# Kernel tuning notes

Hardware: AMD Instinct MI355X
Metric: run time of the kernel (lower is better)

## Reference

```python
import jax, jax.numpy as jnp
import numpy as np

N, C_IN, H, W = 8, 512, 56, 56
CH = 128  # make_divisible(512*0.25, 8)
SCALE = CH ** (-0.5)
BN_EPS = 1e-5


def setup_inputs() -> dict:
    key = jax.random.key(0)
    ks = jax.random.split(key, 6)
    x = jax.random.normal(ks[0], (N, C_IN, H, W), dtype=jnp.float32)
    # 1x1 conv W: in_channels -> 3*channels (with bias)
    W_w = jax.random.normal(ks[1], (3 * CH, C_IN), dtype=jnp.float32) * (2.0 / C_IN) ** 0.5
    W_b = jnp.zeros((3 * CH,), dtype=jnp.float32)
    # 1x1 conv Z: channels -> in_channels (no bias, followed by BN)
    Z_w = jax.random.normal(ks[2], (C_IN, CH), dtype=jnp.float32) * (2.0 / CH) ** 0.5
    bn_gamma = jax.random.normal(ks[3], (C_IN,), dtype=jnp.float32) * 0.1
    bn_beta = jnp.zeros((C_IN,), dtype=jnp.float32)
    bn_mean = jnp.zeros((C_IN,), dtype=jnp.float32)
    bn_var = jnp.ones((C_IN,), dtype=jnp.float32)
    return {"x": x, "W_w": W_w, "W_b": W_b, "Z_w": Z_w,
            "bn_gamma": bn_gamma, "bn_beta": bn_beta,
            "bn_mean": bn_mean, "bn_var": bn_var}


def reference(x, W_w, W_b, Z_w, bn_gamma, bn_beta, bn_mean, bn_var):
    n, c, h, w = x.shape
    xf = x.reshape(n, c, h * w)                               # [N, C, HW]
    proj = jnp.einsum('oc,ncq->noq', W_w, xf) + W_b[None, :, None]  # [N, 3*CH, HW]
    t, p, g = jnp.split(proj, 3, axis=1)                      # each [N, CH, HW]
    s = jnp.einsum('ncq,nck->nqk', t, p)                      # [N, HW, HW]
    s = jax.nn.softmax(s * SCALE, axis=2)
    att = jnp.einsum('nqv,ncv->ncq', s, g)                    # [N, CH, HW]
    z = jnp.einsum('oc,ncq->noq', Z_w, att)                   # [N, C, HW]
    # BatchNorm2d, inference form with running stats
    inv = bn_gamma / jnp.sqrt(bn_var + BN_EPS)
    z = z * inv[None, :, None] + (bn_beta - bn_mean * inv)[None, :, None]
    return z.reshape(n, c, h, w) + x
```

## Files before the change

kernel.cpp:

```cpp
#include <hip/hip_runtime.h>
#include <hip/hip_bf16.h>
#include <math.h>

#define NB    8
#define CIN   512
#define HW    3136
#define CH    128
#define TCH   384
#define SCALE 0.08838834764831845f
#define QKSCALE 0.12751744f
#define BNEPS 1e-5f
#define NSPLIT 4
#define QB    128

typedef __attribute__((ext_vector_type(8)))  short bf16x8;
typedef __attribute__((ext_vector_type(4)))  short bf16x4;
typedef __attribute__((ext_vector_type(4)))  float f32x4;
typedef __attribute__((ext_vector_type(16))) float f32x16;

#define MFMA16(a, b, c) __builtin_amdgcn_mfma_f32_16x16x32_bf16((a), (b), (c), 0, 0, 0)
#define MFMA32(a, b, c) __builtin_amdgcn_mfma_f32_32x32x16_bf16((a), (b), (c), 0, 0, 0)

__device__ inline short f2bf(float f) {
    __hip_bfloat16 h = __float2bfloat16(f);
    return *reinterpret_cast<short*>(&h);
}
__device__ inline unsigned pack2bf(float a, float b) {
    return (unsigned)(unsigned short)f2bf(a) | ((unsigned)(unsigned short)f2bf(b) << 16);
}
__device__ inline float bfraw2f(unsigned short u) {
    return __uint_as_float(((unsigned)u) << 16);
}
__device__ inline float exp2a(float x) {
    float r; asm("v_exp_f32 %0, %1" : "=v"(r) : "v"(x)); return r;
}

__global__ __launch_bounds__(256) void cvt_wts(const float* __restrict__ Ww,
                                               const float* __restrict__ Zw,
                                               __hip_bfloat16* __restrict__ WwB,
                                               __hip_bfloat16* __restrict__ ZwB) {
    const int nW = TCH * CIN / 4;
    const int nZ = CIN * CH / 4;
    int i = blockIdx.x * 256 + threadIdx.x;
    if (i < nW) {
        float4 v = ((const float4*)Ww)[i];
        bf16x4 o; o[0] = f2bf(v.x); o[1] = f2bf(v.y); o[2] = f2bf(v.z); o[3] = f2bf(v.w);
        ((bf16x4*)WwB)[i] = o;
    } else if (i < nW + nZ) {
        int j = i - nW;
        float4 v = ((const float4*)Zw)[j];
        bf16x4 o; o[0] = f2bf(v.x); o[1] = f2bf(v.y); o[2] = f2bf(v.z); o[3] = f2bf(v.w);
        ((bf16x4*)ZwB)[j] = o;
    }
}

__global__ __launch_bounds__(256) void xpose_kernel(const float* __restrict__ x,
                                                    __hip_bfloat16* __restrict__ xT) {
    const int n = blockIdx.z, c0 = blockIdx.y * 64, q0 = blockIdx.x * 64;
    const int tid = threadIdx.x;
    const int mr = tid >> 4, mq = tid & 15;

    __shared__ char T[64 * 128];

    const float* xp = x + ((size_t)(n * CIN + c0 + mr * 4)) * HW + q0 + mq * 4;
    float4 r0 = *(const float4*)(xp);
    float4 r1 = *(const float4*)(xp + HW);
    float4 r2 = *(const float4*)(xp + 2 * HW);
    float4 r3 = *(const float4*)(xp + 3 * HW);
    const float* f0 = (const float*)&r0; const float* f1 = (const float*)&r1;
    const float* f2 = (const float*)&r2; const float* f3 = (const float*)&r3;
#pragma unroll
    for (int j = 0; j < 4; ++j) {
        int q = mq * 4 + j;
        bf16x4 v; v[0] = f2bf(f0[j]); v[1] = f2bf(f1[j]);
                  v[2] = f2bf(f2[j]); v[3] = f2bf(f3[j]);
        *(bf16x4*)(T + q * 128 + ((mr * 8) ^ ((q & 15) << 3))) = v;
    }
    __syncthreads();

    __hip_bfloat16* og = xT + ((size_t)n * HW + q0) * CIN + c0;
#pragma unroll
    for (int it = 0; it < 2; ++it) {
        int ch = it * 256 + tid, rr = ch >> 3, o8 = ch & 7;
        int sw = (rr & 15) << 3;
        bf16x4 lo = *(const bf16x4*)(T + rr * 128 + ((o8 * 16) ^ sw));
        bf16x4 hi = *(const bf16x4*)(T + rr * 128 + ((o8 * 16 + 8) ^ sw));
        bf16x8 v; v[0] = lo[0]; v[1] = lo[1]; v[2] = lo[2]; v[3] = lo[3];
                  v[4] = hi[0]; v[5] = hi[1]; v[6] = hi[2]; v[7] = hi[3];
        *(bf16x8*)(og + (size_t)rr * CIN + o8 * 8) = v;
    }
}

__global__ __launch_bounds__(256) void proj_kernel(const __hip_bfloat16* __restrict__ xT,
                                                   const __hip_bfloat16* __restrict__ WwB,
                                                   const float* __restrict__ Wb,
                                                   __hip_bfloat16* __restrict__ Qt,
                                                   __hip_bfloat16* __restrict__ Kt,
                                                   __hip_bfloat16* __restrict__ Vg) {
    const int n  = blockIdx.z;
    const int m0 = blockIdx.y * 64;
    const int q0 = blockIdx.x * 64;
    const int tid = threadIdx.x;
    const int lane = tid & 63, wv = tid >> 6;
    const int lr = lane & 15, hi = lane >> 4;

    __shared__ char Aw[64 * 128];
    __shared__ char Bx[64 * 128];
    __shared__ char Ts[64 * 128];

    f32x4 acc[4] = {};
    const __hip_bfloat16* xn = xT + ((size_t)n * HW + q0) * CIN;

    for (int k0 = 0; k0 < CIN; k0 += 64) {
#pragma unroll
        for (int it = 0; it < 2; ++it) {
            int ch = it * 256 + tid, r = ch >> 3, o = ch & 7;
            int sw = (o * 16) ^ ((r & 7) << 4);
            bf16x8 a = *(const bf16x8*)(WwB + (size_t)(m0 + r) * CIN + k0 + o * 8);
            *(bf16x8*)(Aw + r * 128 + sw) = a;
            bf16x8 b = *(const bf16x8*)(xn + (size_t)r * CIN + k0 + o * 8);
            *(bf16x8*)(Bx + r * 128 + sw) = b;
        }
        __syncthreads();

        const int mrow = wv * 16 + lr;
#pragma unroll
        for (int ks = 0; ks < 2; ++ks) {
            bf16x8 af = *(const bf16x8*)(Aw + mrow * 128 +
                                         ((ks * 64 + hi * 16) ^ ((mrow & 7) << 4)));
#pragma unroll
            for (int kn = 0; kn < 4; ++kn) {
                int qrow = kn * 16 + lr;
                bf16x8 bfr = *(const bf16x8*)(Bx + qrow * 128 +
                                              ((ks * 64 + hi * 16) ^ ((qrow & 7) << 4)));
                acc[kn] = MFMA16(af, bfr, acc[kn]);
            }
        }
        __syncthreads();
    }

    const int region = m0 >> 7;
    const int c0     = m0 & 127;
    const float oscale = (region == 0) ? QKSCALE : 1.0f;

    float bias[4];
#pragma unroll
    for (int reg = 0; reg < 4; ++reg) bias[reg] = Wb[m0 + wv * 16 + hi * 4 + reg];

#pragma unroll
    for (int kn = 0; kn < 4; ++kn)
#pragma unroll
        for (int reg = 0; reg < 4; ++reg) {
            __hip_bfloat16 v = __float2bfloat16((acc[kn][reg] + bias[reg]) * oscale);
            int row, colb;
            if (region < 2) { row = kn * 16 + lr; colb = (wv * 16 + hi * 4 + reg) * 2; }
            else            { row = wv * 16 + hi * 4 + reg; colb = (kn * 16 + lr) * 2; }
            *(__hip_bfloat16*)(Ts + row * 128 + (colb ^ ((row & 7) << 4))) = v;
        }
    __syncthreads();

    __hip_bfloat16* base;
    size_t rstride;
    if (region == 0)      { base = Qt + (size_t)n * HW * CH + (size_t)q0 * CH + c0; rstride = CH; }
    else if (region == 1) { base = Kt + (size_t)n * HW * CH + (size_t)q0 * CH + c0; rstride = CH; }
    else                  { base = Vg + (size_t)n * CH * HW + (size_t)c0 * HW + q0; rstride = HW; }

#pragma unroll
    for (int it = 0; it < 2; ++it) {
        int ch = it * 256 + tid, rr = ch >> 3, o = ch & 7;
        bf16x8 v = *(const bf16x8*)(Ts + rr * 128 + ((o * 16) ^ ((rr & 7) << 4)));
        *(bf16x8*)(base + (size_t)rr * rstride + o * 8) = v;
    }
}

__global__ __launch_bounds__(256, 2) void attn_kernel(
        const __hip_bfloat16* __restrict__ Qt,
        const __hip_bfloat16* __restrict__ Kt,
        const __hip_bfloat16* __restrict__ Vg,
        __hip_bfloat16* __restrict__ PO,
        float* __restrict__ Mbuf,
        float* __restrict__ Lbuf) {
    const int n = blockIdx.y, s = blockIdx.z;
    const int q0 = blockIdx.x * QB;
    const int tid = threadIdx.x;
    const int lane = tid & 63, wv = tid >> 6;
    const int l31 = lane & 31, h = lane >> 5;

    __shared__ char smem[32768];
    char* Ks = smem;
    char* Vt = smem + 16384;

    const int t0 = (s == 0) ? 0 : (13 + 12 * (s - 1));
    const int t1 = t0 + ((s == 0) ? 13 : 12);

    const __hip_bfloat16* Kg = Kt + (size_t)n * HW * CH;
    const __hip_bfloat16* Vp = Vg + (size_t)n * CH * HW;

    const int qg = q0 + wv * 32 + l31;
    const int qc = (qg < HW) ? qg : (HW - 1);
    const __hip_bfloat16* Qg = Qt + ((size_t)n * HW + qc) * CH + h * 8;
    bf16x8 qf[8];
#pragma unroll
    for (int cs = 0; cs < 8; ++cs) qf[cs] = *(const bf16x8*)(Qg + cs * 16);

    const int kr = tid >> 2, kgb = (tid & 3) * 4;
    const int ksz = (kr & 7) ^ (((kr >> 3) & 1) << 3);
    const int vr = tid >> 1, vgb = (tid & 1) * 4;
    const int vsz = vr & 7;
    const __hip_bfloat16* Ksrc = Kg + (size_t)kr * CH;
    const __hip_bfloat16* Vsrc = Vp + (size_t)vr * HW;
    char* Kd = Ks + kr * 256;
    char* Vd = Vt + vr * 128;

    bf16x8 kreg[4], vreg[4];
    {
        const int kk = t0 * 64;
#pragma unroll
        for (int i = 0; i < 4; ++i)
            kreg[i] = *(const bf16x8*)(Ksrc + (size_t)kk * CH + (kgb + i) * 8);
#pragma unroll
        for (int i = 0; i < 4; ++i)
            vreg[i] = *(const bf16x8*)(Vsrc + kk + (vgb + i) * 8);
    }
#pragma unroll
    for (int i = 0; i < 4; ++i) *(bf16x8*)(Kd + ((kgb + i) ^ ksz) * 16) = kreg[i];
#pragma unroll
    for (int i = 0; i < 4; ++i) *(bf16x8*)(Vd + ((vgb + i) ^ vsz) * 16) = vreg[i];
    __syncthreads();

    const int rsw = (l31 & 7) ^ (((l31 >> 3) & 1) << 3);
    const int vrsw = l31 & 7;

    f32x16 O[4] = {};
    float m_i = -1e30f, l_i = 0.f;

    for (int t = t0; t < t1; ++t) {
        if (t + 1 < t1) {
            const int kk = (t + 1) * 64;
#pragma unroll
            for (int i = 0; i < 4; ++i)
                kreg[i] = *(const bf16x8*)(Ksrc + (size_t)kk * CH + (kgb + i) * 8);
#pragma unroll
            for (int i = 0; i < 4; ++i)
                vreg[i] = *(const bf16x8*)(Vsrc + kk + (vgb + i) * 8);
        }

        f32x16 sa0 = {}, sa1 = {};
#pragma unroll
        for (int cs = 0; cs < 8; ++cs) {
            int goff = ((cs * 2 + h) ^ rsw) * 16;
            bf16x8 k0f = *(const bf16x8*)(Ks + l31 * 256 + goff);
            bf16x8 k1f = *(const bf16x8*)(Ks + (32 + l31) * 256 + goff);
            sa0 = MFMA32(k0f, qf[cs], sa0);
            sa1 = MFMA32(k1f, qf[cs], sa1);
        }

        float pmax = sa0[0];
#pragma unroll
        for (int r = 0; r < 16; ++r) {
            pmax = fmaxf(pmax, sa0[r]);
            pmax = fmaxf(pmax, sa1[r]);
        }
        pmax = fmaxf(pmax, __shfl_xor(pmax, 32));

        if (__any(pmax > m_i)) {
            float nm = fmaxf(m_i, pmax);
            float f  = exp2a(m_i - nm);
            l_i *= f; m_i = nm;
#pragma unroll
            for (int ct = 0; ct < 4; ++ct)
#pragma unroll
                for (int r = 0; r < 16; ++r) O[ct][r] *= f;
        }

        float rs = 0.f;
#pragma unroll
        for (int r = 0; r < 16; ++r) {
            sa0[r] = exp2a(sa0[r] - m_i); rs += sa0[r];
            sa1[r] = exp2a(sa1[r] - m_i); rs += sa1[r];
        }
        rs += __shfl_xor(rs, 32);
        l_i += rs;

        union { unsigned u[4]; bf16x8 v; } pf0, pf1, pf2, pf3;
        {
            unsigned w0 = pack2bf(sa0[0],  sa0[1]),  w1 = pack2bf(sa0[2],  sa0[3]);
            unsigned w2 = pack2bf(sa0[4],  sa0[5]),  w3 = pack2bf(sa0[6],  sa0[7]);
            unsigned w4 = pack2bf(sa0[8],  sa0[9]),  w5 = pack2bf(sa0[10], sa0[11]);
            unsigned w6 = pack2bf(sa0[12], sa0[13]), w7 = pack2bf(sa0[14], sa0[15]);
            unsigned x0 = __shfl_xor((int)w0, 32), x1 = __shfl_xor((int)w1, 32);
            unsigned x2 = __shfl_xor((int)w2, 32), x3 = __shfl_xor((int)w3, 32);
            unsigned x4 = __shfl_xor((int)w4, 32), x5 = __shfl_xor((int)w5, 32);
            unsigned x6 = __shfl_xor((int)w6, 32), x7 = __shfl_xor((int)w7, 32);
            pf0.u[0] = h ? x2 : w0; pf0.u[1] = h ? x3 : w1;
            pf0.u[2] = h ? w2 : x0; pf0.u[3] = h ? w3 : x1;
            pf1.u[0] = h ? x6 : w4; pf1.u[1] = h ? x7 : w5;
            pf1.u[2] = h ? w6 : x4; pf1.u[3] = h ? w7 : x5;
        }
        {
            unsigned w0 = pack2bf(sa1[0],  sa1[1]),  w1 = pack2bf(sa1[2],  sa1[3]);
            unsigned w2 = pack2bf(sa1[4],  sa1[5]),  w3 = pack2bf(sa1[6],  sa1[7]);
            unsigned w4 = pack2bf(sa1[8],  sa1[9]),  w5 = pack2bf(sa1[10], sa1[11]);
            unsigned w6 = pack2bf(sa1[12], sa1[13]), w7 = pack2bf(sa1[14], sa1[15]);
            unsigned x0 = __shfl_xor((int)w0, 32), x1 = __shfl_xor((int)w1, 32);
            unsigned x2 = __shfl_xor((int)w2, 32), x3 = __shfl_xor((int)w3, 32);
            unsigned x4 = __shfl_xor((int)w4, 32), x5 = __shfl_xor((int)w5, 32);
            unsigned x6 = __shfl_xor((int)w6, 32), x7 = __shfl_xor((int)w7, 32);
            pf2.u[0] = h ? x2 : w0; pf2.u[1] = h ? x3 : w1;
            pf2.u[2] = h ? w2 : x0; pf2.u[3] = h ? w3 : x1;
            pf3.u[0] = h ? x6 : w4; pf3.u[1] = h ? x7 : w5;
            pf3.u[2] = h ? w6 : x4; pf3.u[3] = h ? w7 : x5;
        }

#pragma unroll
        for (int ct = 0; ct < 4; ++ct) {
            const char* vrow = Vt + (ct * 32 + l31) * 128;
            bf16x8 v0 = *(const bf16x8*)(vrow + ((0 + h) ^ vrsw) * 16);
            bf16x8 v1 = *(const bf16x8*)(vrow + ((2 + h) ^ vrsw) * 16);
            bf16x8 v2 = *(const bf16x8*)(vrow + ((4 + h) ^ vrsw) * 16);
            bf16x8 v3 = *(const bf16x8*)(vrow + ((6 + h) ^ vrsw) * 16);
            O[ct] = MFMA32(v0, pf0.v, O[ct]);
            O[ct] = MFMA32(v1, pf1.v, O[ct]);
            O[ct] = MFMA32(v2, pf2.v, O[ct]);
            O[ct] = MFMA32(v3, pf3.v, O[ct]);
        }

        __syncthreads();
        if (t + 1 < t1) {
#pragma unroll
            for (int i = 0; i < 4; ++i) *(bf16x8*)(Kd + ((kgb + i) ^ ksz) * 16) = kreg[i];
#pragma unroll
            for (int i = 0; i < 4; ++i) *(bf16x8*)(Vd + ((vgb + i) ^ vsz) * 16) = vreg[i];
        }
        __syncthreads();
    }

    const int qrow = wv * 32 + l31;
    const int esw  = (qrow & 7) << 4;
#pragma unroll
    for (int ct = 0; ct < 4; ++ct)
#pragma unroll
        for (int i = 0; i < 8; ++i) {
            int c = ct * 32 + 2 * (i & 1) + 8 * (i >> 1) + 4 * h;
            unsigned u = pack2bf(O[ct][2 * i], O[ct][2 * i + 1]);
            *(unsigned*)(smem + qrow * 256 + ((c * 2) ^ esw)) = u;
        }
    __syncthreads();
    __hip_bfloat16* pg = PO + ((size_t)(s * NB + n) * HW + q0) * CH;
#pragma unroll
    for (int it = 0; it < 8; ++it) {
        int ch = it * 256 + tid, r = ch >> 4, g = ch & 15;
        if (q0 + r < HW) {
            bf16x8 v = *(const bf16x8*)(smem + r * 256 + ((g * 16) ^ ((r & 7) << 4)));
            *(bf16x8*)(pg + (size_t)r * CH + g * 8) = v;
        }
    }
    if (h == 0 && qg < HW) {
        size_t base = (size_t)(s * NB + n) * HW + qg;
        Mbuf[base] = m_i; Lbuf[base] = l_i;
    }
}

__global__ __launch_bounds__(256) void merge_kernel(
        const __hip_bfloat16* __restrict__ PO,
        const float* __restrict__ Mbuf,
        const float* __restrict__ Lbuf,
        __hip_bfloat16* __restrict__ att) {
    const int idx = blockIdx.x * 256 + threadIdx.x;
    const int nq = idx >> 4;
    const int c0 = (idx & 15) * 8;
    const size_t NHW = (size_t)NB * HW;

    float m[NSPLIT], l[NSPLIT];
#pragma unroll
    for (int s = 0; s < NSPLIT; ++s) { m[s] = Mbuf[s * NHW + nq]; l[s] = Lbuf[s * NHW + nq]; }
    float M = m[0];
#pragma unroll
    for (int s = 1; s < NSPLIT; ++s) M = fmaxf(M, m[s]);
    float w[NSPLIT], denom = 0.f;
#pragma unroll
    for (int s = 0; s < NSPLIT; ++s) { w[s] = exp2f(m[s] - M); denom += w[s] * l[s]; }
    float rinv = 1.f / denom;

    float acc[8] = {};
#pragma unroll
    for (int s = 0; s < NSPLIT; ++s) {
        union { bf16x8 v; unsigned short u[8]; } p;
        p.v = *(const bf16x8*)(PO + (size_t)s * NHW * CH + (size_t)nq * CH + c0);
#pragma unroll
        for (int j = 0; j < 8; ++j) acc[j] += w[s] * bfraw2f(p.u[j]);
    }
    union { bf16x8 v; unsigned short u[8]; } ov;
#pragma unroll
    for (int j = 0; j < 8; ++j) ov.u[j] = (unsigned short)f2bf(acc[j] * rinv);
    *(bf16x8*)(att + (size_t)nq * CH + c0) = ov.v;
}

__global__ __launch_bounds__(256) void zbn_kernel(const __hip_bfloat16* __restrict__ att,
                                                  const __hip_bfloat16* __restrict__ ZwB,
                                                  const float* __restrict__ gamma,
                                                  const float* __restrict__ beta,
                                                  const float* __restrict__ mean,
                                                  const float* __restrict__ var,
                                                  const float* __restrict__ x,
                                                  float* __restrict__ out) {
    const int n  = blockIdx.z;
    const int m0 = blockIdx.y * 64;
    const int q0 = blockIdx.x * 64;
    const int tid = threadIdx.x;
    const int lane = tid & 63, wv = tid >> 6;
    const int lr = lane & 15, hi = lane >> 4;

    __shared__ char smem[32768];
    char* Az = smem;
    char* Ba = smem + 16384;

#pragma unroll
    for (int it = 0; it < 4; ++it) {
        int ch = it * 256 + tid, r = ch >> 4, o = ch & 15;
        int sw = (o * 16) ^ ((r & 7) << 4);
        bf16x8 a = *(const bf16x8*)(ZwB + (size_t)(m0 + r) * CH + o * 8);
        *(bf16x8*)(Az + r * 256 + sw) = a;
        bf16x8 b = *(const bf16x8*)(att + ((size_t)n * HW + q0 + r) * CH + o * 8);
        *(bf16x8*)(Ba + r * 256 + sw) = b;
    }
    __syncthreads();

    f32x4 acc[4] = {};
    const int mrow = wv * 16 + lr;
#pragma unroll
    for (int ks = 0; ks < 4; ++ks) {
        bf16x8 af = *(const bf16x8*)(Az + mrow * 256 +
                                     ((ks * 64 + hi * 16) ^ ((mrow & 7) << 4)));
#pragma unroll
        for (int kn = 0; kn < 4; ++kn) {
            int qrow = kn * 16 + lr;
            bf16x8 bfr = *(const bf16x8*)(Ba + qrow * 256 +
                                          ((ks * 64 + hi * 16) ^ ((qrow & 7) << 4)));
            acc[kn] = MFMA16(af, bfr, acc[kn]);
        }
    }
    __syncthreads();

    float inv[4], add[4];
#pragma unroll
    for (int reg = 0; reg < 4; ++reg) {
        int m = m0 + wv * 16 + hi * 4 + reg;
        inv[reg] = gamma[m] * rsqrtf(var[m] + BNEPS);
        add[reg] = beta[m] - mean[m] * inv[reg];
    }

#pragma unroll
    for (int kn = 0; kn < 4; ++kn)
#pragma unroll
        for (int reg = 0; reg < 4; ++reg) {
            int row = wv * 16 + hi * 4 + reg;
            int colb = (kn * 16 + lr) * 4;
            *(float*)(smem + row * 256 + (colb ^ ((row & 7) << 4))) =
                acc[kn][reg] * inv[reg] + add[reg];
        }
    __syncthreads();

#pragma unroll
    for (int it = 0; it < 4; ++it) {
        int ch = it * 256 + tid, rr = ch >> 4, o = ch & 15;
        f32x4 v = *(const f32x4*)(smem + rr * 256 + ((o * 16) ^ ((rr & 7) << 4)));
        size_t idx = (size_t)n * CIN * HW + (size_t)(m0 + rr) * HW + q0 + o * 4;
        float4 xv = *(const float4*)(x + idx);
        float4 ov; ov.x = v[0] + xv.x; ov.y = v[1] + xv.y;
                   ov.z = v[2] + xv.z; ov.w = v[3] + xv.w;
        *(float4*)(out + idx) = ov;
    }
}

extern "C" void kernel_launch(void* const* d_in, const int* in_sizes, int n_in,
                              void* d_out, int out_size, void* d_ws, size_t ws_size,
                              hipStream_t stream) {
    const float* x     = (const float*)d_in[0];
    const float* Ww    = (const float*)d_in[1];
    const float* Wb    = (const float*)d_in[2];
    const float* Zw    = (const float*)d_in[3];
    const float* gamma = (const float*)d_in[4];
    const float* beta  = (const float*)d_in[5];
    const float* mean  = (const float*)d_in[6];
    const float* var   = (const float*)d_in[7];
    float* out = (float*)d_out;

    const size_t xT_bytes  = (size_t)NB * HW * CIN * 2;
    const size_t qkv_bytes = (size_t)NB * HW * CH * 2;
    char* ob = (char*)d_out;
    __hip_bfloat16* xT  = (__hip_bfloat16*)ob;
    __hip_bfloat16* Qt  = (__hip_bfloat16*)(ob + xT_bytes);
    __hip_bfloat16* Kt  = (__hip_bfloat16*)(ob + xT_bytes + qkv_bytes);
    __hip_bfloat16* Vgb = (__hip_bfloat16*)(ob + xT_bytes + 2 * qkv_bytes);
    __hip_bfloat16* PO  = (__hip_bfloat16*)ob;

    char* w = (char*)d_ws;
    __hip_bfloat16* attb = (__hip_bfloat16*)w;                       w += qkv_bytes;
    __hip_bfloat16* WwB  = (__hip_bfloat16*)w;                       w += (size_t)TCH * CIN * 2;
    __hip_bfloat16* ZwB  = (__hip_bfloat16*)w;                       w += (size_t)CIN * CH * 2;
    float* Mbuf = (float*)w;                                         w += (size_t)NSPLIT * NB * HW * 4;
    float* Lbuf = (float*)w;

    cvt_wts<<<dim3(256), 256, 0, stream>>>(Ww, Zw, WwB, ZwB);
    xpose_kernel<<<dim3(HW / 64, CIN / 64, NB), 256, 0, stream>>>(x, xT);
    proj_kernel<<<dim3(HW / 64, TCH / 64, NB), 256, 0, stream>>>(xT, WwB, Wb, Qt, Kt, Vgb);
    attn_kernel<<<dim3((HW + QB - 1) / QB, NB, NSPLIT), 256, 0, stream>>>(Qt, Kt, Vgb,
                                                                          PO, Mbuf, Lbuf);
    merge_kernel<<<dim3(NB * HW * 16 / 256), 256, 0, stream>>>(PO, Mbuf, Lbuf, attb);
    zbn_kernel<<<dim3(HW / 64, CIN / 64, NB), 256, 0, stream>>>(attb, ZwB, gamma, beta,
                                                                mean, var, x, out);
}
```

Before: 150.8 us.

## Widen projection tile to 128 rows, use permlane32 swap and MFMA priority in attention

The projection kernel now computes 128 output channels per block instead of 64, so each x tile loaded into shared memory is reused across twice as many MFMAs and half as many blocks are launched. In the attention loop, the cross-half shuffles used to build the P operand are replaced by v_permlane32_swap_b32, which avoids the LDS-backed shuffles and the select instructions. The MFMA sections are also wrapped in s_setprio raises so waves issuing matrix ops get scheduling priority. In exchange, the projection kernel uses more registers and LDS per block, and the epilogue is serialized over two halves with extra barriers.

```diff
diff --git a/kernel.cpp b/kernel.cpp
--- a/kernel.cpp
+++ b/kernel.cpp
@@ -98,78 +98,87 @@
                                                    __hip_bfloat16* __restrict__ Kt,
                                                    __hip_bfloat16* __restrict__ Vg) {
     const int n  = blockIdx.z;
-    const int m0 = blockIdx.y * 64;
+    const int m0 = blockIdx.y * 128;
     const int q0 = blockIdx.x * 64;
     const int tid = threadIdx.x;
     const int lane = tid & 63, wv = tid >> 6;
     const int lr = lane & 15, hi = lane >> 4;
 
-    __shared__ char Aw[64 * 128];
+    __shared__ char Aw[128 * 128];
     __shared__ char Bx[64 * 128];
     __shared__ char Ts[64 * 128];
 
-    f32x4 acc[4] = {};
+    f32x4 acc[2][4] = {};
     const __hip_bfloat16* xn = xT + ((size_t)n * HW + q0) * CIN;
 
     for (int k0 = 0; k0 < CIN; k0 += 64) {
+#pragma unroll
+        for (int it = 0; it < 4; ++it) {
+            int ch = it * 256 + tid, r = ch >> 3, o = ch & 7;
+            bf16x8 a = *(const bf16x8*)(WwB + (size_t)(m0 + r) * CIN + k0 + o * 8);
+            *(bf16x8*)(Aw + r * 128 + ((o * 16) ^ ((r & 7) << 4))) = a;
+        }
 #pragma unroll
         for (int it = 0; it < 2; ++it) {
             int ch = it * 256 + tid, r = ch >> 3, o = ch & 7;
-            int sw = (o * 16) ^ ((r & 7) << 4);
-            bf16x8 a = *(const bf16x8*)(WwB + (size_t)(m0 + r) * CIN + k0 + o * 8);
-            *(bf16x8*)(Aw + r * 128 + sw) = a;
             bf16x8 b = *(const bf16x8*)(xn + (size_t)r * CIN + k0 + o * 8);
-            *(bf16x8*)(Bx + r * 128 + sw) = b;
+            *(bf16x8*)(Bx + r * 128 + ((o * 16) ^ ((r & 7) << 4))) = b;
         }
         __syncthreads();
 
-        const int mrow = wv * 16 + lr;
 #pragma unroll
         for (int ks = 0; ks < 2; ++ks) {
-            bf16x8 af = *(const bf16x8*)(Aw + mrow * 128 +
-                                         ((ks * 64 + hi * 16) ^ ((mrow & 7) << 4)));
-#pragma unroll
-            for (int kn = 0; kn < 4; ++kn) {
-                int qrow = kn * 16 + lr;
-                bf16x8 bfr = *(const bf16x8*)(Bx + qrow * 128 +
-                                              ((ks * 64 + hi * 16) ^ ((qrow & 7) << 4)));
-                acc[kn] = MFMA16(af, bfr, acc[kn]);
+#pragma unroll
+            for (int half = 0; half < 2; ++half) {
+                const int mrow = half * 64 + wv * 16 + lr;
+                bf16x8 af = *(const bf16x8*)(Aw + mrow * 128 +
+                                             ((ks * 64 + hi * 16) ^ ((mrow & 7) << 4)));
+#pragma unroll
+                for (int kn = 0; kn < 4; ++kn) {
+                    int qrow = kn * 16 + lr;
+                    bf16x8 bfr = *(const bf16x8*)(Bx + qrow * 128 +
+                                                  ((ks * 64 + hi * 16) ^ ((qrow & 7) << 4)));
+                    acc[half][kn] = MFMA16(af, bfr, acc[half][kn]);
+                }
             }
         }
         __syncthreads();
     }
 
-    const int region = m0 >> 7;
-    const int c0     = m0 & 127;
-    const float oscale = (region == 0) ? QKSCALE : 1.0f;
-
-    float bias[4];
-#pragma unroll
-    for (int reg = 0; reg < 4; ++reg) bias[reg] = Wb[m0 + wv * 16 + hi * 4 + reg];
-
-#pragma unroll
-    for (int kn = 0; kn < 4; ++kn)
-#pragma unroll
-        for (int reg = 0; reg < 4; ++reg) {
-            __hip_bfloat16 v = __float2bfloat16((acc[kn][reg] + bias[reg]) * oscale);
-            int row, colb;
-            if (region < 2) { row = kn * 16 + lr; colb = (wv * 16 + hi * 4 + reg) * 2; }
-            else            { row = wv * 16 + hi * 4 + reg; colb = (kn * 16 + lr) * 2; }
-            *(__hip_bfloat16*)(Ts + row * 128 + (colb ^ ((row & 7) << 4))) = v;
-        }
-    __syncthreads();
-
-    __hip_bfloat16* base;
-    size_t rstride;
-    if (region == 0)      { base = Qt + (size_t)n * HW * CH + (size_t)q0 * CH + c0; rstride = CH; }
-    else if (region == 1) { base = Kt + (size_t)n * HW * CH + (size_t)q0 * CH + c0; rstride = CH; }
-    else                  { base = Vg + (size_t)n * CH * HW + (size_t)c0 * HW + q0; rstride = HW; }
-
-#pragma unroll
-    for (int it = 0; it < 2; ++it) {
-        int ch = it * 256 + tid, rr = ch >> 3, o = ch & 7;
-        bf16x8 v = *(const bf16x8*)(Ts + rr * 128 + ((o * 16) ^ ((rr & 7) << 4)));
-        *(bf16x8*)(base + (size_t)rr * rstride + o * 8) = v;
+#pragma unroll
+    for (int half = 0; half < 2; ++half) {
+        const int mbase  = m0 + half * 64;
+        const int region = mbase >> 7;
+        const int c0     = mbase & 127;
+        const float oscale = (region == 0) ? QKSCALE : 1.0f;
+
+#pragma unroll
+        for (int kn = 0; kn < 4; ++kn)
+#pragma unroll
+            for (int reg = 0; reg < 4; ++reg) {
+                float bias = Wb[mbase + wv * 16 + hi * 4 + reg];
+                __hip_bfloat16 v =
+                    __float2bfloat16((acc[half][kn][reg] + bias) * oscale);
+                int row, colb;
+                if (region < 2) { row = kn * 16 + lr; colb = (wv * 16 + hi * 4 + reg) * 2; }
+                else            { row = wv * 16 + hi * 4 + reg; colb = (kn * 16 + lr) * 2; }
+                *(__hip_bfloat16*)(Ts + row * 128 + (colb ^ ((row & 7) << 4))) = v;
+            }
+        __syncthreads();
+
+        __hip_bfloat16* base;
+        size_t rstride;
+        if (region == 0)      { base = Qt + (size_t)n * HW * CH + (size_t)q0 * CH + c0; rstride = CH; }
+        else if (region == 1) { base = Kt + (size_t)n * HW * CH + (size_t)q0 * CH + c0; rstride = CH; }
+        else                  { base = Vg + (size_t)n * CH * HW + (size_t)c0 * HW + q0; rstride = HW; }
+
+#pragma unroll
+        for (int it = 0; it < 2; ++it) {
+            int ch = it * 256 + tid, rr = ch >> 3, o = ch & 7;
+            bf16x8 v = *(const bf16x8*)(Ts + rr * 128 + ((o * 16) ^ ((rr & 7) << 4)));
+            *(bf16x8*)(base + (size_t)rr * rstride + o * 8) = v;
+        }
+        __syncthreads();
     }
 }
 
@@ -246,6 +255,7 @@
         }
 
         f32x16 sa0 = {}, sa1 = {};
+        __builtin_amdgcn_s_setprio(1);
 #pragma unroll
         for (int cs = 0; cs < 8; ++cs) {
             int goff = ((cs * 2 + h) ^ rsw) * 16;
@@ -254,6 +264,7 @@
             sa0 = MFMA32(k0f, qf[cs], sa0);
             sa1 = MFMA32(k1f, qf[cs], sa1);
         }
+        __builtin_amdgcn_s_setprio(0);
 
         float pmax = sa0[0];
 #pragma unroll
@@ -288,30 +299,27 @@
             unsigned w2 = pack2bf(sa0[4],  sa0[5]),  w3 = pack2bf(sa0[6],  sa0[7]);
             unsigned w4 = pack2bf(sa0[8],  sa0[9]),  w5 = pack2bf(sa0[10], sa0[11]);
             unsigned w6 = pack2bf(sa0[12], sa0[13]), w7 = pack2bf(sa0[14], sa0[15]);
-            unsigned x0 = __shfl_xor((int)w0, 32), x1 = __shfl_xor((int)w1, 32);
-            unsigned x2 = __shfl_xor((int)w2, 32), x3 = __shfl_xor((int)w3, 32);
-            unsigned x4 = __shfl_xor((int)w4, 32), x5 = __shfl_xor((int)w5, 32);
-            unsigned x6 = __shfl_xor((int)w6, 32), x7 = __shfl_xor((int)w7, 32);
-            pf0.u[0] = h ? x2 : w0; pf0.u[1] = h ? x3 : w1;
-            pf0.u[2] = h ? w2 : x0; pf0.u[3] = h ? w3 : x1;
-            pf1.u[0] = h ? x6 : w4; pf1.u[1] = h ? x7 : w5;
-            pf1.u[2] = h ? w6 : x4; pf1.u[3] = h ? w7 : x5;
+            asm("v_permlane32_swap_b32 %0, %1" : "+v"(w0), "+v"(w2));
+            asm("v_permlane32_swap_b32 %0, %1" : "+v"(w1), "+v"(w3));
+            asm("v_permlane32_swap_b32 %0, %1" : "+v"(w4), "+v"(w6));
+            asm("v_permlane32_swap_b32 %0, %1" : "+v"(w5), "+v"(w7));
+            pf0.u[0] = w0; pf0.u[1] = w1; pf0.u[2] = w2; pf0.u[3] = w3;
+            pf1.u[0] = w4; pf1.u[1] = w5; pf1.u[2] = w6; pf1.u[3] = w7;
         }
         {
             unsigned w0 = pack2bf(sa1[0],  sa1[1]),  w1 = pack2bf(sa1[2],  sa1[3]);
             unsigned w2 = pack2bf(sa1[4],  sa1[5]),  w3 = pack2bf(sa1[6],  sa1[7]);
             unsigned w4 = pack2bf(sa1[8],  sa1[9]),  w5 = pack2bf(sa1[10], sa1[11]);
             unsigned w6 = pack2bf(sa1[12], sa1[13]), w7 = pack2bf(sa1[14], sa1[15]);
-            unsigned x0 = __shfl_xor((int)w0, 32), x1 = __shfl_xor((int)w1, 32);
-            unsigned x2 = __shfl_xor((int)w2, 32), x3 = __shfl_xor((int)w3, 32);
-            unsigned x4 = __shfl_xor((int)w4, 32), x5 = __shfl_xor((int)w5, 32);
-            unsigned x6 = __shfl_xor((int)w6, 32), x7 = __shfl_xor((int)w7, 32);
-            pf2.u[0] = h ? x2 : w0; pf2.u[1] = h ? x3 : w1;
-            pf2.u[2] = h ? w2 : x0; pf2.u[3] = h ? w3 : x1;
-            pf3.u[0] = h ? x6 : w4; pf3.u[1] = h ? x7 : w5;
-            pf3.u[2] = h ? w6 : x4; pf3.u[3] = h ? w7 : x5;
-        }
-
+            asm("v_permlane32_swap_b32 %0, %1" : "+v"(w0), "+v"(w2));
+            asm("v_permlane32_swap_b32 %0, %1" : "+v"(w1), "+v"(w3));
+            asm("v_permlane32_swap_b32 %0, %1" : "+v"(w4), "+v"(w6));
+            asm("v_permlane32_swap_b32 %0, %1" : "+v"(w5), "+v"(w7));
+            pf2.u[0] = w0; pf2.u[1] = w1; pf2.u[2] = w2; pf2.u[3] = w3;
+            pf3.u[0] = w4; pf3.u[1] = w5; pf3.u[2] = w6; pf3.u[3] = w7;
+        }
+
+        __builtin_amdgcn_s_setprio(1);
 #pragma unroll
         for (int ct = 0; ct < 4; ++ct) {
             const char* vrow = Vt + (ct * 32 + l31) * 128;
@@ -324,6 +332,7 @@
             O[ct] = MFMA32(v2, pf2.v, O[ct]);
             O[ct] = MFMA32(v3, pf3.v, O[ct]);
         }
+        __builtin_amdgcn_s_setprio(0);
 
         __syncthreads();
         if (t + 1 < t1) {
@@ -504,7 +513,7 @@
 
     cvt_wts<<<dim3(256), 256, 0, stream>>>(Ww, Zw, WwB, ZwB);
     xpose_kernel<<<dim3(HW / 64, CIN / 64, NB), 256, 0, stream>>>(x, xT);
-    proj_kernel<<<dim3(HW / 64, TCH / 64, NB), 256, 0, stream>>>(xT, WwB, Wb, Qt, Kt, Vgb);
+    proj_kernel<<<dim3(HW / 64, TCH / 128, NB), 256, 0, stream>>>(xT, WwB, Wb, Qt, Kt, Vgb);
     attn_kernel<<<dim3((HW + QB - 1) / QB, NB, NSPLIT), 256, 0, stream>>>(Qt, Kt, Vgb,
                                                                           PO, Mbuf, Lbuf);
     merge_kernel<<<dim3(NB * HW * 16 / 256), 256, 0, stream>>>(PO, Mbuf, Lbuf, attb);
```

Result: slower. 155.0 us (+2.8%).
